# Optimization experiments

Measured on AMD Instinct MI355X. Metric: run time of the kernel, lower is better.

The kernel has to match this reference:

```python
import jax, jax.numpy as jnp
import numpy as np

N_NODES = 10000
DEG = 32            # max_edges (fixed degree after padding)
CHANNELS = 16
IN_DIM = 4
BATCH = 8


def setup_inputs() -> dict:
    key = jax.random.key(0)
    k1, k2, k3 = jax.random.split(key, 3)
    E = N_NODES * DEG
    x = jax.random.normal(k1, (BATCH, N_NODES, IN_DIM), dtype=jnp.float32)
    # neighbor indices in [0, N_NODES]; index N_NODES is the padded 'useless' zero node
    edges = jax.random.randint(k2, (E,), 0, N_NODES + 1, dtype=jnp.int64)
    # torch.rand init: uniform [0,1); one weight tensor per input channel
    weights = jax.random.uniform(k3, (IN_DIM, E, CHANNELS), dtype=jnp.float32)
    return {"x": x, "edges": edges, "weights": weights}


def reference(x, edges, weights):
    B, N, in_dim = x.shape
    E = edges.shape[0]
    deg = E // N
    C = weights.shape[-1]
    # append zero 'useless node' so padding index N gathers zeros
    x_pad = jnp.concatenate([x, jnp.zeros((B, 1, in_dim), dtype=x.dtype)], axis=1)  # [B, N+1, in_dim]
    # super_edges = cat([edges]*C); viewed as [E, C] row-major (matches torch .view)
    idx = jnp.tile(edges, C).reshape(E, C)  # [E, C]
    out = jnp.zeros((B, N, C), dtype=x.dtype)
    for i in range(in_dim):  # small fixed loop over input channels (distinct weights)
        g = x_pad[:, :, i]              # [B, N+1]
        toc = g[:, idx]                 # gather -> [B, E, C]
        conv = toc * weights[i]         # per-edge weights broadcast over batch
        out = out + conv.reshape(B, N, deg, C).sum(axis=2)  # fixed-window segment sum
    return out
```

## Files before the change

kernel.cpp:

```cpp
#include <hip/hip_runtime.h>
#include <hip/hip_bf16.h>

#define N_NODES 10000
#define DEG     32
#define CH      16
#define IN_DIM  4
#define BATCH   8
#define E_EDGES (N_NODES * DEG)
#define WI_STRIDE (E_EDGES * CH)
#define P_COUNT 625
#define LX_STRIDE 36

__global__ __launch_bounds__(256) void lcg_transpose(const float* __restrict__ x,
                                                     float* __restrict__ xt) {
    int t = blockIdx.x * 256 + threadIdx.x;
    if (t < BATCH * N_NODES) {
        int b = t / N_NODES;
        int node = t - b * N_NODES;
        float4 v = *(const float4*)(x + 4 * t);
        *(float4*)(xt + node * 32 + b * 4) = v;
    } else if (t < BATCH * N_NODES + 8) {
        int r = t - BATCH * N_NODES;
        *(float4*)(xt + N_NODES * 32 + r * 4) = make_float4(0.f, 0.f, 0.f, 0.f);
    }
}

__global__ __launch_bounds__(256, 2) void lcg_main(
    const float* __restrict__ xt,
    const int*   __restrict__ edges,
    const float* __restrict__ w,
    float*       __restrict__ out)
{
    __shared__ float lx[512 * LX_STRIDE];

    int p = blockIdx.x;
    int t = threadIdx.x;

    {
        int sub = t & 7;
        int rg  = t >> 3;
        const int* ep = edges + 512 * p;
        int nd[16];
#pragma unroll
        for (int k = 0; k < 16; k++) nd[k] = ep[rg + 32 * k];
#pragma unroll
        for (int k = 0; k < 16; k++) {
            int s = rg + 32 * k;
            float4 v = *(const float4*)(xt + nd[k] * 32 + sub * 4);
            *(float4*)(&lx[s * LX_STRIDE + sub * 4]) = v;
        }
    }
    __syncthreads();

    int c = t & 15;
    int j = t >> 4;
    int n = p + P_COUNT * j;

    const float* wp = w + (n * DEG) * CH + c;
    float acc[BATCH];
#pragma unroll
    for (int b = 0; b < BATCH; b++) acc[b] = 0.0f;

#pragma unroll 2
    for (int d = 0; d < DEG; d++) {
        float w0 = __builtin_nontemporal_load(wp + d * CH);
        float w1 = __builtin_nontemporal_load(wp + d * CH + WI_STRIDE);
        float w2 = __builtin_nontemporal_load(wp + d * CH + 2 * WI_STRIDE);
        float w3 = __builtin_nontemporal_load(wp + d * CH + 3 * WI_STRIDE);
        const float* lp = &lx[(16 * d + c) * LX_STRIDE];
        float4 xv[BATCH];
#pragma unroll
        for (int b = 0; b < BATCH; b++) xv[b] = *(const float4*)(lp + 4 * b);
#pragma unroll
        for (int b = 0; b < BATCH; b++)
            acc[b] += xv[b].x * w0 + xv[b].y * w1 + xv[b].z * w2 + xv[b].w * w3;
    }

    int ob = n * CH + c;
#pragma unroll
    for (int b = 0; b < BATCH; b++)
        __builtin_nontemporal_store(acc[b], out + b * (N_NODES * CH) + ob);
}

extern "C" void kernel_launch(void* const* d_in, const int* in_sizes, int n_in,
                              void* d_out, int out_size, void* d_ws, size_t ws_size,
                              hipStream_t stream) {
    const float* x     = (const float*)d_in[0];
    const int*   edges = (const int*)d_in[1];
    const float* w     = (const float*)d_in[2];
    float* out = (float*)d_out;
    float* xt  = (float*)d_ws;

    int tr_total  = BATCH * N_NODES + 8;
    int tr_blocks = (tr_total + 255) / 256;
    lcg_transpose<<<tr_blocks, 256, 0, stream>>>(x, xt);

    lcg_main<<<P_COUNT, 256, 0, stream>>>(xt, edges, w, out);
}
```

Baseline: 141.0 us.

## Remap threads to channel-quad × batch-pair for vectorized weight loads and stores

New measurement: 141.2 us. No clear change (+0.1%).

```diff
diff --git a/kernel.cpp b/kernel.cpp
--- a/kernel.cpp
+++ b/kernel.cpp
@@ -52,34 +52,42 @@
     }
     __syncthreads();
 
-    int c = t & 15;
-    int j = t >> 4;
-    int n = p + P_COUNT * j;
+    int cq = t & 3;
+    int j  = (t >> 2) & 15;
+    int bq = t >> 6;
+    int n  = p + P_COUNT * j;
 
-    const float* wp = w + (n * DEG) * CH + c;
-    float acc[BATCH];
-#pragma unroll
-    for (int b = 0; b < BATCH; b++) acc[b] = 0.0f;
+    const float* wb = w + n * (DEG * CH) + 4 * cq;
+    float accA[4] = {0.f, 0.f, 0.f, 0.f};
+    float accB[4] = {0.f, 0.f, 0.f, 0.f};
 
 #pragma unroll 2
     for (int d = 0; d < DEG; d++) {
-        float w0 = __builtin_nontemporal_load(wp + d * CH);
-        float w1 = __builtin_nontemporal_load(wp + d * CH + WI_STRIDE);
-        float w2 = __builtin_nontemporal_load(wp + d * CH + 2 * WI_STRIDE);
-        float w3 = __builtin_nontemporal_load(wp + d * CH + 3 * WI_STRIDE);
-        const float* lp = &lx[(16 * d + c) * LX_STRIDE];
-        float4 xv[BATCH];
-#pragma unroll
-        for (int b = 0; b < BATCH; b++) xv[b] = *(const float4*)(lp + 4 * b);
-#pragma unroll
-        for (int b = 0; b < BATCH; b++)
-            acc[b] += xv[b].x * w0 + xv[b].y * w1 + xv[b].z * w2 + xv[b].w * w3;
+        float4 w0 = *(const float4*)(wb + d * CH);
+        float4 w1 = *(const float4*)(wb + d * CH + WI_STRIDE);
+        float4 w2 = *(const float4*)(wb + d * CH + 2 * WI_STRIDE);
+        float4 w3 = *(const float4*)(wb + d * CH + 3 * WI_STRIDE);
+        const float* lrow = &lx[(16 * d + 4 * cq) * LX_STRIDE + 8 * bq];
+
+#define CC_STEP(cc, s0, s1, s2, s3)                                         \
+        {                                                                   \
+            float4 xa = *(const float4*)(lrow + (cc) * LX_STRIDE);          \
+            float4 xb = *(const float4*)(lrow + (cc) * LX_STRIDE + 4);      \
+            accA[cc] += xa.x * (s0) + xa.y * (s1) + xa.z * (s2) + xa.w * (s3); \
+            accB[cc] += xb.x * (s0) + xb.y * (s1) + xb.z * (s2) + xb.w * (s3); \
+        }
+        CC_STEP(0, w0.x, w1.x, w2.x, w3.x)
+        CC_STEP(1, w0.y, w1.y, w2.y, w3.y)
+        CC_STEP(2, w0.z, w1.z, w2.z, w3.z)
+        CC_STEP(3, w0.w, w1.w, w2.w, w3.w)
+#undef CC_STEP
     }
 
-    int ob = n * CH + c;
-#pragma unroll
-    for (int b = 0; b < BATCH; b++)
-        __builtin_nontemporal_store(acc[b], out + b * (N_NODES * CH) + ob);
+    int ob = n * CH + 4 * cq;
+    *(float4*)(out + (2 * bq + 0) * (N_NODES * CH) + ob) =
+        make_float4(accA[0], accA[1], accA[2], accA[3]);
+    *(float4*)(out + (2 * bq + 1) * (N_NODES * CH) + ob) =
+        make_float4(accB[0], accB[1], accB[2], accB[3]);
 }
 
 extern "C" void kernel_launch(void* const* d_in, const int* in_sizes, int n_in,
```

## Split each node's degree loop across four lanes with 1024-thread blocks

Applied to the files above, without the earlier changes.

New measurement: 129.6 us. 8.1% less time.

```diff
diff --git a/kernel.cpp b/kernel.cpp
--- a/kernel.cpp
+++ b/kernel.cpp
@@ -25,7 +25,7 @@
     }
 }
 
-__global__ __launch_bounds__(256, 2) void lcg_main(
+__global__ __launch_bounds__(1024, 8) void lcg_main(
     const float* __restrict__ xt,
     const int*   __restrict__ edges,
     const float* __restrict__ w,
@@ -40,46 +40,55 @@
         int sub = t & 7;
         int rg  = t >> 3;
         const int* ep = edges + 512 * p;
-        int nd[16];
+        int nd[4];
 #pragma unroll
-        for (int k = 0; k < 16; k++) nd[k] = ep[rg + 32 * k];
+        for (int k = 0; k < 4; k++) nd[k] = ep[rg + 128 * k];
 #pragma unroll
-        for (int k = 0; k < 16; k++) {
-            int s = rg + 32 * k;
+        for (int k = 0; k < 4; k++) {
+            int s = rg + 128 * k;
             float4 v = *(const float4*)(xt + nd[k] * 32 + sub * 4);
             *(float4*)(&lx[s * LX_STRIDE + sub * 4]) = v;
         }
     }
     __syncthreads();
 
-    int c = t & 15;
-    int j = t >> 4;
-    int n = p + P_COUNT * j;
+    int lane = t & 63;
+    int j    = t >> 6;
+    int c    = lane & 15;
+    int dq   = lane >> 4;
+    int n    = p + P_COUNT * j;
 
-    const float* wp = w + (n * DEG) * CH + c;
+    const float* wb = w + n * (DEG * CH) + lane;
+
     float acc[BATCH];
 #pragma unroll
     for (int b = 0; b < BATCH; b++) acc[b] = 0.0f;
 
-#pragma unroll 2
-    for (int d = 0; d < DEG; d++) {
-        float w0 = __builtin_nontemporal_load(wp + d * CH);
-        float w1 = __builtin_nontemporal_load(wp + d * CH + WI_STRIDE);
-        float w2 = __builtin_nontemporal_load(wp + d * CH + 2 * WI_STRIDE);
-        float w3 = __builtin_nontemporal_load(wp + d * CH + 3 * WI_STRIDE);
-        const float* lp = &lx[(16 * d + c) * LX_STRIDE];
-        float4 xv[BATCH];
+    const float* lrow = &lx[(16 * dq + c) * LX_STRIDE];
+
+#pragma unroll 1
+    for (int ds = 0; ds < 8; ds++) {
+        float w0 = wb[64 * ds];
+        float w1 = wb[64 * ds + WI_STRIDE];
+        float w2 = wb[64 * ds + 2 * WI_STRIDE];
+        float w3 = wb[64 * ds + 3 * WI_STRIDE];
+        const float* lr = lrow + ds * (64 * LX_STRIDE);
 #pragma unroll
-        for (int b = 0; b < BATCH; b++) xv[b] = *(const float4*)(lp + 4 * b);
+        for (int b = 0; b < BATCH; b++) {
+            float4 xq = *(const float4*)(lr + 4 * b);
+            acc[b] += xq.x * w0 + xq.y * w1 + xq.z * w2 + xq.w * w3;
+        }
+    }
+
 #pragma unroll
-        for (int b = 0; b < BATCH; b++)
-            acc[b] += xv[b].x * w0 + xv[b].y * w1 + xv[b].z * w2 + xv[b].w * w3;
+    for (int b = 0; b < BATCH; b++) {
+        acc[b] += __shfl_xor(acc[b], 16, 64);
+        acc[b] += __shfl_xor(acc[b], 32, 64);
     }
 
     int ob = n * CH + c;
-#pragma unroll
-    for (int b = 0; b < BATCH; b++)
-        __builtin_nontemporal_store(acc[b], out + b * (N_NODES * CH) + ob);
+    out[(2 * dq + 0) * (N_NODES * CH) + ob] = acc[2 * dq + 0];
+    out[(2 * dq + 1) * (N_NODES * CH) + ob] = acc[2 * dq + 1];
 }
 
 extern "C" void kernel_launch(void* const* d_in, const int* in_sizes, int n_in,
@@ -95,5 +104,5 @@
     int tr_blocks = (tr_total + 255) / 256;
     lcg_transpose<<<tr_blocks, 256, 0, stream>>>(x, xt);
 
-    lcg_main<<<P_COUNT, 256, 0, stream>>>(xt, edges, w, out);
+    lcg_main<<<P_COUNT, 1024, 0, stream>>>(xt, edges, w, out);
 }
```
